# Performance work log

Hardware: AMD Instinct MI355X
Metric: run time of the kernel (lower is better)

Reference implementation:

```python
import jax, jax.numpy as jnp
import numpy as np

TEMPERATURE = 0.07
BASE_TEMPERATURE = 0.07


def setup_inputs() -> dict:
    key = jax.random.key(0)
    k1, k2 = jax.random.split(key)
    features = jax.random.normal(k1, (4096, 2, 128), dtype=jnp.float32)
    labels = jax.random.randint(k2, (4096,), 0, 100, dtype=jnp.int64)
    return {"features": features, "labels": labels}


def reference(features, labels):
    # features: [B, n_views, D], labels: [B]
    B, n_views, D = features.shape
    N = B * n_views

    # label equality mask [B, B]
    lab = labels.reshape(-1, 1)
    mask = (lab == lab.T).astype(jnp.float32)

    # flatten views (C-order, same as torch .view) and L2-normalize
    feat = features.reshape(N, D)
    feat = feat / jnp.clip(jnp.linalg.norm(feat, axis=1, keepdims=True), 1e-12)

    # similarity logits [N, N]
    logits = jnp.matmul(feat, feat.T) / TEMPERATURE
    logits_max = jax.lax.stop_gradient(jnp.max(logits, axis=1, keepdims=True))
    logits = logits - logits_max

    # tile mask to [N, N] (torch .repeat ordering) and remove self-contrast
    mask = jnp.tile(mask, (n_views, n_views))
    logits_mask = 1.0 - jnp.eye(N, dtype=jnp.float32)
    mask = mask * logits_mask

    exp_logits = jnp.exp(logits) * logits_mask
    log_prob = logits - jnp.log(jnp.sum(exp_logits, axis=1, keepdims=True) + 1e-12)

    mask_pos_pairs = jnp.clip(jnp.sum(mask, axis=1), 1.0)
    mean_log_prob_pos = jnp.sum(mask * log_prob, axis=1) / mask_pos_pairs

    loss = -(TEMPERATURE / BASE_TEMPERATURE) * mean_log_prob_pos
    return jnp.mean(loss.reshape(n_views, B))
```

## Files before the change

### kernel.cpp

```cpp
#include <hip/hip_runtime.h>
#include <hip/hip_bf16.h>
#include <hip/hip_fp8.h>
#include <math.h>

#define NB 4096
#define NN 8192
#define DD 128
#define NCLS 100
#define NSPLIT 32

constexpr float INV_T = 14.285714285714286f;
constexpr float EC1   = 20.609929155556620f;
constexpr float EC0   = -20.609929155556620f;
constexpr float LN2   = 0.6931471805599453f;

typedef unsigned char u8;
typedef __attribute__((ext_vector_type(8))) int   v8i;
typedef __attribute__((ext_vector_type(4))) int   v4i;
typedef __attribute__((ext_vector_type(4))) float f32x4;


__global__ __launch_bounds__(256) void k_norm(const float* __restrict__ feat,
                                              u8* __restrict__ fb8,
                                              float* __restrict__ selfdot,
                                              float* __restrict__ out) {
    const int gid = blockIdx.x * 256 + threadIdx.x;
    if (gid == 0) out[0] = 0.0f;
    const int r    = gid >> 6;
    const int lane = threadIdx.x & 63;
    const float2 v = ((const float2*)(feat + (size_t)r * DD))[lane];
    float ss = v.x * v.x + v.y * v.y;
#pragma unroll
    for (int off = 1; off < 64; off <<= 1) ss += __shfl_xor(ss, off, 64);
    const float scale = 1.0f / fmaxf(sqrtf(ss), 1e-12f);
    const __hip_fp8_e4m3 qx(v.x * scale), qy(v.y * scale);
    const unsigned short pack = (unsigned short)qx.__x |
                                ((unsigned short)qy.__x << 8);
    const int g    = r >> 4;
    const int n15r = r & 15;
    const int qc   = lane >> 4;
    const int hc   = (lane >> 3) & 1;
    const int bofs = (2 * lane) & 15;
    *(unsigned short*)(fb8 + (size_t)g * 2048 + hc * 1024 +
                       ((qc * 16 + n15r) << 4) + bofs) = pack;
    const float xb = (float)qx, yb = (float)qy;
    float s2 = xb * xb + yb * yb;
#pragma unroll
    for (int off = 1; off < 64; off <<= 1) s2 += __shfl_xor(s2, off, 64);
    if (lane == 0) selfdot[r] = s2;
}

__global__ __launch_bounds__(256, 4) void k_main(const u8* __restrict__ fb8,
                                                 const int* __restrict__ labels,
                                                 float* __restrict__ g_se,
                                                 float* __restrict__ g_ps) {
    __shared__ int slab[256];

    const int tid  = threadIdx.x;
    const int lane = tid & 63;
    const int w    = tid >> 6;
    const int rb   = blockIdx.x >> 5;
    const int js   = blockIdx.x & (NSPLIT - 1);
    const int i0   = rb * 128 + w * 32;
    const int jb0  = js * 256;
    const int q    = lane >> 4;
    const int n15  = lane & 15;

    slab[tid] = labels[(jb0 + tid) & (NB - 1)];

    v8i af[2];
#pragma unroll
    for (int tt = 0; tt < 2; ++tt) {
        const u8* ap = fb8 + (size_t)((i0 >> 4) + tt) * 2048 + lane * 16;
        const v4i lo = *(const v4i*)ap;
        const v4i hi = *(const v4i*)(ap + 1024);
        v8i a;
#pragma unroll
        for (int k = 0; k < 4; ++k) { a[k] = lo[k]; a[4 + k] = hi[k]; }
        af[tt] = a;
    }
    int labi[8];
#pragma unroll
    for (int tt = 0; tt < 2; ++tt)
#pragma unroll
        for (int r = 0; r < 4; ++r)
            labi[tt * 4 + r] = labels[(i0 + tt * 16 + q * 4 + r) & (NB - 1)];

    float a_se[8] = {}, a_ps[8] = {};

    __syncthreads();

    const u8* bbase = fb8 + (size_t)(jb0 >> 4) * 2048 + lane * 16;
#pragma unroll 4
    for (int jt = 0; jt < 16; ++jt) {
        const u8* bp = bbase + (size_t)jt * 2048;
        const v4i lo = *(const v4i*)bp;
        const v4i hi = *(const v4i*)(bp + 1024);
        v8i bb;
#pragma unroll
        for (int k = 0; k < 4; ++k) { bb[k] = lo[k]; bb[4 + k] = hi[k]; }
        const int labj = slab[jt * 16 + n15];
        f32x4 a0 = {0.f, 0.f, 0.f, 0.f}, a1 = {0.f, 0.f, 0.f, 0.f};
        a0 = __builtin_amdgcn_mfma_scale_f32_16x16x128_f8f6f4(
                 af[0], bb, a0, 0, 0, 0, 0x7F7F7F7F, 0, 0x7F7F7F7F);
        a1 = __builtin_amdgcn_mfma_scale_f32_16x16x128_f8f6f4(
                 af[1], bb, a1, 0, 0, 0, 0x7F7F7F7F, 0, 0x7F7F7F7F);
#pragma unroll
        for (int r = 0; r < 4; ++r) {
            const float d0 = a0[r], d1 = a1[r];
            a_se[r]     += __builtin_amdgcn_exp2f(fmaf(d0, EC1, EC0));
            a_se[4 + r] += __builtin_amdgcn_exp2f(fmaf(d1, EC1, EC0));
            a_ps[r]     += (labi[r]     == labj) ? d0 : 0.0f;
            a_ps[4 + r] += (labi[4 + r] == labj) ? d1 : 0.0f;
        }
    }

#pragma unroll
    for (int s = 0; s < 8; ++s) {
        float v1 = a_se[s], v2 = a_ps[s];
#pragma unroll
        for (int off = 1; off < 16; off <<= 1) {
            v1 += __shfl_xor(v1, off, 64);
            v2 += __shfl_xor(v2, off, 64);
        }
        if (n15 == 0) {
            const int row = i0 + (s >> 2) * 16 + q * 4 + (s & 3);
            g_se[js * NN + row] = v1;
            g_ps[js * NN + row] = v2;
        }
    }
}

__global__ __launch_bounds__(256) void k_final(const int* __restrict__ labels,
                                               const float* __restrict__ g_se,
                                               const float* __restrict__ g_ps,
                                               const float* __restrict__ selfdot,
                                               float* __restrict__ out) {
    __shared__ int hist[NCLS];
    const int tid = threadIdx.x;
    for (int i = tid; i < NCLS; i += 256) hist[i] = 0;
    __syncthreads();
    for (int b = tid; b < NB; b += 256) atomicAdd(&hist[labels[b]], 1);
    __syncthreads();

    const int r = blockIdx.x * 256 + tid;
    const int c = labels[r & (NB - 1)];
    float se = 0.f, ps = 0.f;
#pragma unroll
    for (int t = 0; t < NSPLIT; ++t) {
        se += g_se[t * NN + r];
        ps += g_ps[t * NN + r];
    }
    const float sd = selfdot[r];
    se -= __builtin_amdgcn_exp2f(fmaf(sd, EC1, EC0));
    const float ct = (float)(2 * hist[c] - 1);
    const float possum = INV_T * ((ps - sd) - ct);
    const float lg  = __builtin_amdgcn_logf(se + 1e-12f) * LN2;
    const float mlpp = (possum - ct * lg) / fmaxf(ct, 1.0f);
    float v = -mlpp * (1.0f / (float)NN);
#pragma unroll
    for (int off = 1; off < 64; off <<= 1) v += __shfl_xor(v, off, 64);
    __shared__ float sred[4];
    if ((tid & 63) == 0) sred[tid >> 6] = v;
    __syncthreads();
    if (tid == 0) atomicAdd(out, sred[0] + sred[1] + sred[2] + sred[3]);
}

extern "C" void kernel_launch(void* const* d_in, const int* in_sizes, int n_in,
                              void* d_out, int out_size, void* d_ws, size_t ws_size,
                              hipStream_t stream) {
    const float* feat = (const float*)d_in[0];
    const int* labels = (const int*)d_in[1];
    float* out        = (float*)d_out;
    char* ws          = (char*)d_ws;

    u8* fb8         = (u8*)ws;
    float* g_se     = (float*)(ws + (size_t)1 * 1024 * 1024);
    float* g_ps     = g_se + NSPLIT * NN;
    float* selfdot  = g_ps + NSPLIT * NN;

    k_norm<<<NN / 4, 256, 0, stream>>>(feat, fb8, selfdot, out);
    k_main<<<(NN / 128) * NSPLIT, 256, 0, stream>>>(fb8, labels, g_se, g_ps);
    k_final<<<NN / 256, 256, 0, stream>>>(labels, g_se, g_ps, selfdot, out);
}
```

Baseline: 95.02 us.

## Double row tile per wave and transpose partial-sum layout for vectorized final reduce

Each wave now computes 64 rows (four 16-row MFMA tiles) against each B tile instead of 32, halving the grid and the B-fragment reloads per row. Row labels are staged through shared memory rather than loaded individually from global. Partial sums are stored row-major ([row][split]) so the final kernel reads them with float4 loads. The larger tile raises register pressure (16 accumulators each for se and ps), and the grid drops to 1024 blocks, so occupancy and latency hiding may suffer.

```diff
diff --git a/kernel.cpp b/kernel.cpp
--- a/kernel.cpp
+++ b/kernel.cpp
@@ -55,22 +55,24 @@
                                                  float* __restrict__ g_se,
                                                  float* __restrict__ g_ps) {
     __shared__ int slab[256];
+    __shared__ int rlab[256];
 
     const int tid  = threadIdx.x;
     const int lane = tid & 63;
     const int w    = tid >> 6;
     const int rb   = blockIdx.x >> 5;
     const int js   = blockIdx.x & (NSPLIT - 1);
-    const int i0   = rb * 128 + w * 32;
+    const int i0   = rb * 256 + w * 64;
     const int jb0  = js * 256;
     const int q    = lane >> 4;
     const int n15  = lane & 15;
 
     slab[tid] = labels[(jb0 + tid) & (NB - 1)];
+    rlab[tid] = labels[(rb * 256 + tid) & (NB - 1)];
 
-    v8i af[2];
+    v8i af[4];
 #pragma unroll
-    for (int tt = 0; tt < 2; ++tt) {
+    for (int tt = 0; tt < 4; ++tt) {
         const u8* ap = fb8 + (size_t)((i0 >> 4) + tt) * 2048 + lane * 16;
         const v4i lo = *(const v4i*)ap;
         const v4i hi = *(const v4i*)(ap + 1024);
@@ -79,19 +81,20 @@
         for (int k = 0; k < 4; ++k) { a[k] = lo[k]; a[4 + k] = hi[k]; }
         af[tt] = a;
     }
-    int labi[8];
-#pragma unroll
-    for (int tt = 0; tt < 2; ++tt)
-#pragma unroll
-        for (int r = 0; r < 4; ++r)
-            labi[tt * 4 + r] = labels[(i0 + tt * 16 + q * 4 + r) & (NB - 1)];
-
-    float a_se[8] = {}, a_ps[8] = {};
 
     __syncthreads();
 
+    int labi[16];
+#pragma unroll
+    for (int tt = 0; tt < 4; ++tt)
+#pragma unroll
+        for (int r = 0; r < 4; ++r)
+            labi[tt * 4 + r] = rlab[w * 64 + tt * 16 + q * 4 + r];
+
+    float a_se[16] = {}, a_ps[16] = {};
+
     const u8* bbase = fb8 + (size_t)(jb0 >> 4) * 2048 + lane * 16;
-#pragma unroll 4
+#pragma unroll 2
     for (int jt = 0; jt < 16; ++jt) {
         const u8* bp = bbase + (size_t)jt * 2048;
         const v4i lo = *(const v4i*)bp;
@@ -100,23 +103,22 @@
 #pragma unroll
         for (int k = 0; k < 4; ++k) { bb[k] = lo[k]; bb[4 + k] = hi[k]; }
         const int labj = slab[jt * 16 + n15];
-        f32x4 a0 = {0.f, 0.f, 0.f, 0.f}, a1 = {0.f, 0.f, 0.f, 0.f};
-        a0 = __builtin_amdgcn_mfma_scale_f32_16x16x128_f8f6f4(
-                 af[0], bb, a0, 0, 0, 0, 0x7F7F7F7F, 0, 0x7F7F7F7F);
-        a1 = __builtin_amdgcn_mfma_scale_f32_16x16x128_f8f6f4(
-                 af[1], bb, a1, 0, 0, 0, 0x7F7F7F7F, 0, 0x7F7F7F7F);
 #pragma unroll
-        for (int r = 0; r < 4; ++r) {
-            const float d0 = a0[r], d1 = a1[r];
-            a_se[r]     += __builtin_amdgcn_exp2f(fmaf(d0, EC1, EC0));
-            a_se[4 + r] += __builtin_amdgcn_exp2f(fmaf(d1, EC1, EC0));
-            a_ps[r]     += (labi[r]     == labj) ? d0 : 0.0f;
-            a_ps[4 + r] += (labi[4 + r] == labj) ? d1 : 0.0f;
+        for (int tt = 0; tt < 4; ++tt) {
+            const f32x4 z = {0.f, 0.f, 0.f, 0.f};
+            const f32x4 d = __builtin_amdgcn_mfma_scale_f32_16x16x128_f8f6f4(
+                     af[tt], bb, z, 0, 0, 0, 0x7F7F7F7F, 0, 0x7F7F7F7F);
+#pragma unroll
+            for (int r = 0; r < 4; ++r) {
+                const float dv = d[r];
+                a_se[tt * 4 + r] += __builtin_amdgcn_exp2f(fmaf(dv, EC1, EC0));
+                a_ps[tt * 4 + r] += (labi[tt * 4 + r] == labj) ? dv : 0.0f;
+            }
         }
     }
 
 #pragma unroll
-    for (int s = 0; s < 8; ++s) {
+    for (int s = 0; s < 16; ++s) {
         float v1 = a_se[s], v2 = a_ps[s];
 #pragma unroll
         for (int off = 1; off < 16; off <<= 1) {
@@ -125,8 +127,8 @@
         }
         if (n15 == 0) {
             const int row = i0 + (s >> 2) * 16 + q * 4 + (s & 3);
-            g_se[js * NN + row] = v1;
-            g_ps[js * NN + row] = v2;
+            g_se[row * NSPLIT + js] = v1;
+            g_ps[row * NSPLIT + js] = v2;
         }
     }
 }
@@ -145,11 +147,15 @@
 
     const int r = blockIdx.x * 256 + tid;
     const int c = labels[r & (NB - 1)];
+    const float4* pse = (const float4*)(g_se + (size_t)r * NSPLIT);
+    const float4* pps = (const float4*)(g_ps + (size_t)r * NSPLIT);
     float se = 0.f, ps = 0.f;
 #pragma unroll
-    for (int t = 0; t < NSPLIT; ++t) {
-        se += g_se[t * NN + r];
-        ps += g_ps[t * NN + r];
+    for (int t = 0; t < NSPLIT / 4; ++t) {
+        const float4 a = pse[t];
+        const float4 b = pps[t];
+        se += (a.x + a.y) + (a.z + a.w);
+        ps += (b.x + b.y) + (b.z + b.w);
     }
     const float sd = selfdot[r];
     se -= __builtin_amdgcn_exp2f(fmaf(sd, EC1, EC0));
@@ -180,6 +186,6 @@
     float* selfdot  = g_ps + NSPLIT * NN;
 
     k_norm<<<NN / 4, 256, 0, stream>>>(feat, fb8, selfdot, out);
-    k_main<<<(NN / 128) * NSPLIT, 256, 0, stream>>>(fb8, labels, g_se, g_ps);
+    k_main<<<(NN / 256) * NSPLIT, 256, 0, stream>>>(fb8, labels, g_se, g_ps);
     k_final<<<NN / 256, 256, 0, stream>>>(labels, g_se, g_ps, selfdot, out);
 }
```

Result: faster. 87.77 us (-7.6%).
